# Performance work log

Hardware: AMD Instinct MI355X
Metric: run time of the kernel (lower is better)

Reference implementation:

```python
import jax, jax.numpy as jnp
import numpy as np

BN_EPS = 1e-5


def setup_inputs() -> dict:
    key = jax.random.key(0)
    ks = jax.random.split(key, 8)
    b, c, h, w, d = 16, 256, 128, 128, 64
    x = jax.random.normal(ks[0], (b, c, h, w), dtype=jnp.float32)
    conv1_w = jax.random.normal(ks[1], (c, c), dtype=jnp.float32) * np.sqrt(2.0 / c)
    conv1_b = jax.random.normal(ks[2], (c,), dtype=jnp.float32) * 0.02
    mk_w = jax.random.normal(ks[3], (d, c), dtype=jnp.float32) * np.sqrt(2.0 / d)
    mv_w = jnp.transpose(mk_w)  # original ties mv.weight = mk.weight.permute(1,0,2)
    conv2_w = jax.random.normal(ks[4], (c, c), dtype=jnp.float32) * np.sqrt(2.0 / c)
    bn_gamma = jnp.ones((c,), dtype=jnp.float32)
    bn_beta = jnp.zeros((c,), dtype=jnp.float32)
    bn_mean = jax.random.normal(ks[5], (c,), dtype=jnp.float32) * 0.1
    bn_var = jax.random.uniform(ks[6], (c,), dtype=jnp.float32, minval=0.5, maxval=1.5)
    return {"x": x, "conv1_w": conv1_w, "conv1_b": conv1_b, "mk_w": mk_w,
            "mv_w": mv_w, "conv2_w": conv2_w, "bn_gamma": bn_gamma,
            "bn_beta": bn_beta, "bn_mean": bn_mean, "bn_var": bn_var}


def reference(x, conv1_w, conv1_b, mk_w, mv_w, conv2_w, bn_gamma, bn_beta, bn_mean, bn_var):
    b, c, h, w = x.shape
    n = h * w
    identity = x
    # conv1: 1x1 conv with bias -> [b, c, n]
    y = jnp.einsum('oc,bchw->bohw', conv1_w, x) + conv1_b[None, :, None, None]
    y = y.reshape(b, c, n)
    # external attention: mk projection [b, d, n]
    attn = jnp.einsum('dc,bcn->bdn', mk_w, y)
    attn = jax.nn.softmax(attn, axis=-1)              # softmax over spatial N
    attn = attn / (1e-9 + attn.sum(axis=1, keepdims=True))  # column-normalize over d
    # mv projection back to channels [b, c, n]
    z = jnp.einsum('cd,bdn->bcn', mv_w, attn)
    z = z.reshape(b, c, h, w)
    # conv2 (1x1, no bias) + BatchNorm (inference) + residual + relu
    z = jnp.einsum('oc,bchw->bohw', conv2_w, z)
    inv = bn_gamma / jnp.sqrt(bn_var + BN_EPS)
    z = z * inv[None, :, None, None] + (bn_beta - bn_mean * inv)[None, :, None, None]
    return jax.nn.relu(z + identity)
```

## Files before the change

### kernel.cpp

```cpp
#include <hip/hip_runtime.h>
#include <hip/hip_bf16.h>

#define HW 16384
#define C  256
#define D  64
#define NB 16
#define M0 16.0f

typedef unsigned short u16;
typedef __attribute__((ext_vector_type(4))) float  f32x4;
typedef __attribute__((ext_vector_type(4))) short  s16x4;
typedef __attribute__((ext_vector_type(8))) short  s16x8;

__device__ __forceinline__ float bf2f(u16 u) {
    return __uint_as_float(((unsigned int)u) << 16);
}
__device__ __forceinline__ short f2bfs(float f) {
    union { __hip_bfloat16 h; short s; } u;
    u.h = __float2bfloat16(f);
    return u.s;
}
__device__ __forceinline__ u16 f2bf(float f) {
    unsigned int u = __float_as_uint(f);
    unsigned int r = (u + 0x7fffu + ((u >> 16) & 1u)) >> 16;
    return (u16)r;
}

#define MFMA16(a, b, c) __builtin_amdgcn_mfma_f32_16x16x32_bf16((a), (b), (c), 0, 0, 0)

__global__ void precompute_kernel(const float* __restrict__ conv1_w,
                                  const float* __restrict__ conv1_b,
                                  const float* __restrict__ mk_w,
                                  const float* __restrict__ mv_w,
                                  const float* __restrict__ conv2_w,
                                  const float* __restrict__ gamma,
                                  const float* __restrict__ beta,
                                  const float* __restrict__ mean,
                                  const float* __restrict__ var,
                                  short* __restrict__ Ath,
                                  short* __restrict__ Atl,
                                  float* __restrict__ amk,
                                  short* __restrict__ Bmb,
                                  float* __restrict__ shift,
                                  float* __restrict__ esum)
{
    int gid = blockIdx.x * blockDim.x + threadIdx.x;
    if (gid < C * D) {
        int d = gid >> 8, cp = gid & 255;
        float s = 0.f;
        for (int c = 0; c < C; ++c) s += mk_w[d * C + c] * conv1_w[c * C + cp];
        u16 h = f2bf(s);
        Ath[gid] = (short)h;
        Atl[gid] = (short)f2bf(s - bf2f(h));
    } else if (gid < 2 * C * D) {
        int g = gid - C * D;
        int o = g >> 6, d = g & 63;
        float inv = gamma[o] * rsqrtf(var[o] + 1e-5f);
        float s = 0.f;
        for (int c = 0; c < C; ++c) s += conv2_w[o * C + c] * mv_w[c * D + d];
        Bmb[g] = (short)f2bf(s * inv);
    } else if (gid < 2 * C * D + D) {
        int d = gid - 2 * C * D;
        float s = 0.f;
        for (int c = 0; c < C; ++c) s += mk_w[d * C + c] * conv1_b[c];
        amk[d] = s;
    } else if (gid < 2 * C * D + D + C) {
        int o = gid - (2 * C * D + D);
        float inv = gamma[o] * rsqrtf(var[o] + 1e-5f);
        shift[o] = beta[o] - mean[o] * inv;
    } else if (gid < 2 * C * D + D + C + NB * D) {
        esum[gid - (2 * C * D + D + C)] = 0.f;
    }
}

#define NT1 64
#define XR  (C + 8)
__global__ __launch_bounds__(256, 3) void pexp_kernel(const float* __restrict__ x,
                                                      const short* __restrict__ Ath,
                                                      const short* __restrict__ Atl,
                                                      const float* __restrict__ amk,
                                                      u16* __restrict__ pexp,
                                                      float* __restrict__ esum)
{
    __shared__ short xs[NT1 * XR];
    const int t = threadIdx.x;
    const int b = blockIdx.y;
    const int n0 = blockIdx.x * NT1;
    const int lane = t & 63, w = t >> 6;
    const int col = lane & 15, g = lane >> 4;

    const float* xb = x + (size_t)b * C * HW + n0;
    #pragma unroll
    for (int i = 0; i < 4; ++i) {
        int cell = i * 256 + t;
        int nq = cell & 15, cq = cell >> 4;
        int c0 = cq * 4, nn = nq * 4;
        const float* gp = xb + (size_t)c0 * HW + nn;
        f32x4 r0 = *(const f32x4*)(gp);
        f32x4 r1 = *(const f32x4*)(gp + HW);
        f32x4 r2 = *(const f32x4*)(gp + 2 * HW);
        f32x4 r3 = *(const f32x4*)(gp + 3 * HW);
        #pragma unroll
        for (int j = 0; j < 4; ++j) {
            s16x4 hi = { f2bfs(r0[j]), f2bfs(r1[j]), f2bfs(r2[j]), f2bfs(r3[j]) };
            *(s16x4*)&xs[(nn + j) * XR + c0] = hi;
        }
    }
    __syncthreads();

    s16x8 Ah[8], Al[8];
    {
        const short* ah = Ath + (size_t)(w * 16 + col) * C + 8 * g;
        const short* al = Atl + (size_t)(w * 16 + col) * C + 8 * g;
        #pragma unroll
        for (int ks = 0; ks < 8; ++ks) {
            Ah[ks] = *(const s16x8*)(ah + ks * 32);
            Al[ks] = *(const s16x8*)(al + ks * 32);
        }
    }

    f32x4 zz = {0.f, 0.f, 0.f, 0.f};
    f32x4 acc[4] = { zz, zz, zz, zz };
    #pragma unroll
    for (int ks = 0; ks < 8; ++ks) {
        #pragma unroll
        for (int nt = 0; nt < 4; ++nt) {
            s16x8 xf = *(const s16x8*)&xs[(nt * 16 + col) * XR + ks * 32 + 8 * g];
            acc[nt] = MFMA16(xf, Ah[ks], acc[nt]);
            acc[nt] = MFMA16(xf, Al[ks], acc[nt]);
        }
    }

    const float am = amk[w * 16 + col];
    u16* pb = pexp + (size_t)b * D * HW + (size_t)(w * 16 + col) * HW + n0;
    float rs = 0.f;
    #pragma unroll
    for (int nt = 0; nt < 4; ++nt) {
        s16x4 st4;
        #pragma unroll
        for (int r = 0; r < 4; ++r) {
            float e = exp2f((acc[nt][r] + am - M0) * 1.44269504088896340736f);
            rs += e;
            st4[r] = f2bfs(e);
        }
        *(s16x4*)(pb + nt * 16 + 4 * g) = st4;
    }
    rs += __shfl_xor(rs, 16);
    rs += __shfl_xor(rs, 32);
    if (lane < 16) atomicAdd(esum + b * D + w * 16 + lane, rs);
}

#define NT3 64
__global__ __launch_bounds__(256, 3) void out_kernel(const float* __restrict__ x,
                                                     const u16* __restrict__ pexp,
                                                     const float* __restrict__ esum,
                                                     const short* __restrict__ Bmb,
                                                     const float* __restrict__ shift,
                                                     float* __restrict__ out)
{
    __shared__ short ps[NT3 * 72];
    __shared__ float csum[4][NT3];
    __shared__ float rr[NT3];

    const int t = threadIdx.x;
    const int b  = (NB - 1) - blockIdx.y;
    const int n0 = ((int)gridDim.x - 1 - blockIdx.x) * NT3;

    {
        const int nl = t & 63, dq = t >> 6;
        const u16* lg = pexp + (size_t)b * D * HW + (size_t)(dq * 16) * HW + n0 + nl;
        const float* es = esum + b * D + dq * 16;
        float cs = 0.f;
        #pragma unroll
        for (int j4 = 0; j4 < 4; ++j4) {
            s16x4 pk;
            #pragma unroll
            for (int jj = 0; jj < 4; ++jj) {
                int j = j4 * 4 + jj;
                float iv = __fdividef(1.0f, es[j]);
                float pv = bf2f(lg[(size_t)j * HW]) * iv;
                cs += pv;
                pk[jj] = f2bfs(pv);
            }
            *(s16x4*)&ps[nl * 72 + dq * 16 + j4 * 4] = pk;
        }
        csum[dq][nl] = cs;
    }
    __syncthreads();
    if (t < NT3)
        rr[t] = __fdividef(1.0f, csum[0][t] + csum[1][t] + csum[2][t] + csum[3][t] + 1e-9f);
    __syncthreads();

    const int lane = t & 63, col = lane & 15, g = lane >> 4;
    const int w = t >> 6;

    s16x8 Bf[4][2];
    #pragma unroll
    for (int ot = 0; ot < 4; ++ot) {
        const short* bp = Bmb + (size_t)(w * 64 + ot * 16 + col) * D + 8 * g;
        Bf[ot][0] = *(const s16x8*)(bp);
        Bf[ot][1] = *(const s16x8*)(bp + 32);
    }

    f32x4 zz = {0.f, 0.f, 0.f, 0.f};
    f32x4 acc[4][4];
    #pragma unroll
    for (int ot = 0; ot < 4; ++ot)
        #pragma unroll
        for (int nt = 0; nt < 4; ++nt) acc[ot][nt] = zz;

    #pragma unroll
    for (int nt = 0; nt < 4; ++nt) {
        const short* pr = &ps[(nt * 16 + col) * 72 + 8 * g];
        s16x8 p0 = *(const s16x8*)(pr);
        s16x8 p1 = *(const s16x8*)(pr + 32);
        #pragma unroll
        for (int ot = 0; ot < 4; ++ot) {
            acc[ot][nt] = MFMA16(p0, Bf[ot][0], acc[ot][nt]);
            acc[ot][nt] = MFMA16(p1, Bf[ot][1], acc[ot][nt]);
        }
    }

    float sh[4];
    #pragma unroll
    for (int ot = 0; ot < 4; ++ot) sh[ot] = shift[w * 64 + ot * 16 + col];

    const float* xb = x + (size_t)b * C * HW + n0;
    float* ob = out + (size_t)b * C * HW + n0;
    #pragma unroll
    for (int nt = 0; nt < 4; ++nt) {
        f32x4 rv = *(const f32x4*)&rr[nt * 16 + 4 * g];
        #pragma unroll
        for (int ot = 0; ot < 4; ++ot) {
            const size_t off = (size_t)(w * 64 + ot * 16 + col) * HW + nt * 16 + 4 * g;
            f32x4 xv = *(const f32x4*)(xb + off);
            f32x4 vv;
            #pragma unroll
            for (int r = 0; r < 4; ++r)
                vv[r] = fmaxf(acc[ot][nt][r] * rv[r] + sh[ot] + xv[r], 0.f);
            __builtin_nontemporal_store(vv, (f32x4*)(ob + off));
        }
    }
}

extern "C" void kernel_launch(void* const* d_in, const int* in_sizes, int n_in,
                              void* d_out, int out_size, void* d_ws, size_t ws_size,
                              hipStream_t stream)
{
    const float* x       = (const float*)d_in[0];
    const float* conv1_w = (const float*)d_in[1];
    const float* conv1_b = (const float*)d_in[2];
    const float* mk_w    = (const float*)d_in[3];
    const float* mv_w    = (const float*)d_in[4];
    const float* conv2_w = (const float*)d_in[5];
    const float* gamma   = (const float*)d_in[6];
    const float* beta    = (const float*)d_in[7];
    const float* mean    = (const float*)d_in[8];
    const float* var     = (const float*)d_in[9];
    float* out = (float*)d_out;

    float* amk   = (float*)d_ws;
    float* shift = amk + D;
    float* esum  = shift + C;
    short* Ath   = (short*)(esum + NB * D);
    short* Atl   = Ath + C * D;
    short* Bmb   = Atl + C * D;
    u16* pexp    = (u16*)(Bmb + C * D);

    const int pre_work = 2 * C * D + D + C + NB * D;
    precompute_kernel<<<(pre_work + 255) / 256, 256, 0, stream>>>(
        conv1_w, conv1_b, mk_w, mv_w, conv2_w, gamma, beta, mean, var,
        Ath, Atl, amk, Bmb, shift, esum);

    pexp_kernel<<<dim3(HW / NT1, NB), 256, 0, stream>>>(x, Ath, Atl, amk, pexp, esum);

    out_kernel<<<dim3(HW / NT3, NB), 256, 0, stream>>>(x, pexp, esum, Bmb, shift, out);
}
```

Before: 544.2 us.

## Recompute attention logits in output kernel instead of materializing pexp buffer

```diff
diff --git a/kernel.cpp b/kernel.cpp
--- a/kernel.cpp
+++ b/kernel.cpp
@@ -6,6 +6,7 @@
 #define D  64
 #define NB 16
 #define M0 16.0f
+#define LOG2E 1.44269504088896340736f
 
 typedef unsigned short u16;
 typedef __attribute__((ext_vector_type(4))) float  f32x4;
@@ -75,11 +76,10 @@
 
 #define NT1 64
 #define XR  (C + 8)
-__global__ __launch_bounds__(256, 3) void pexp_kernel(const float* __restrict__ x,
+__global__ __launch_bounds__(256, 3) void esum_kernel(const float* __restrict__ x,
                                                       const short* __restrict__ Ath,
                                                       const short* __restrict__ Atl,
                                                       const float* __restrict__ amk,
-                                                      u16* __restrict__ pexp,
                                                       float* __restrict__ esum)
 {
     __shared__ short xs[NT1 * XR];
@@ -132,19 +132,12 @@
     }
 
     const float am = amk[w * 16 + col];
-    u16* pb = pexp + (size_t)b * D * HW + (size_t)(w * 16 + col) * HW + n0;
     float rs = 0.f;
     #pragma unroll
-    for (int nt = 0; nt < 4; ++nt) {
-        s16x4 st4;
-        #pragma unroll
-        for (int r = 0; r < 4; ++r) {
-            float e = exp2f((acc[nt][r] + am - M0) * 1.44269504088896340736f);
-            rs += e;
-            st4[r] = f2bfs(e);
-        }
-        *(s16x4*)(pb + nt * 16 + 4 * g) = st4;
-    }
+    for (int nt = 0; nt < 4; ++nt)
+        #pragma unroll
+        for (int r = 0; r < 4; ++r)
+            rs += exp2f((acc[nt][r] + am - M0) * LOG2E);
     rs += __shfl_xor(rs, 16);
     rs += __shfl_xor(rs, 32);
     if (lane < 16) atomicAdd(esum + b * D + w * 16 + lane, rs);
@@ -152,12 +145,15 @@
 
 #define NT3 64
 __global__ __launch_bounds__(256, 3) void out_kernel(const float* __restrict__ x,
-                                                     const u16* __restrict__ pexp,
+                                                     const short* __restrict__ Ath,
+                                                     const short* __restrict__ Atl,
+                                                     const float* __restrict__ amk,
                                                      const float* __restrict__ esum,
                                                      const short* __restrict__ Bmb,
                                                      const float* __restrict__ shift,
                                                      float* __restrict__ out)
 {
+    __shared__ short xs[NT3 * XR];
     __shared__ short ps[NT3 * 72];
     __shared__ float csum[4][NT3];
     __shared__ float rr[NT3];
@@ -165,34 +161,76 @@
     const int t = threadIdx.x;
     const int b  = (NB - 1) - blockIdx.y;
     const int n0 = ((int)gridDim.x - 1 - blockIdx.x) * NT3;
+    const int lane = t & 63, w = t >> 6;
+    const int col = lane & 15, g = lane >> 4;
+
+    const float* xb = x + (size_t)b * C * HW + n0;
+    #pragma unroll
+    for (int i = 0; i < 4; ++i) {
+        int cell = i * 256 + t;
+        int nq = cell & 15, cq = cell >> 4;
+        int c0 = cq * 4, nn = nq * 4;
+        const float* gp = xb + (size_t)c0 * HW + nn;
+        f32x4 r0 = *(const f32x4*)(gp);
+        f32x4 r1 = *(const f32x4*)(gp + HW);
+        f32x4 r2 = *(const f32x4*)(gp + 2 * HW);
+        f32x4 r3 = *(const f32x4*)(gp + 3 * HW);
+        #pragma unroll
+        for (int j = 0; j < 4; ++j) {
+            s16x4 hi = { f2bfs(r0[j]), f2bfs(r1[j]), f2bfs(r2[j]), f2bfs(r3[j]) };
+            *(s16x4*)&xs[(nn + j) * XR + c0] = hi;
+        }
+    }
+    __syncthreads();
+
+    {
+        s16x8 Ah[8], Al[8];
+        const short* ah = Ath + (size_t)(w * 16 + col) * C + 8 * g;
+        const short* al = Atl + (size_t)(w * 16 + col) * C + 8 * g;
+        #pragma unroll
+        for (int ks = 0; ks < 8; ++ks) {
+            Ah[ks] = *(const s16x8*)(ah + ks * 32);
+            Al[ks] = *(const s16x8*)(al + ks * 32);
+        }
+
+        f32x4 zz = {0.f, 0.f, 0.f, 0.f};
+        f32x4 acc[4] = { zz, zz, zz, zz };
+        #pragma unroll
+        for (int ks = 0; ks < 8; ++ks) {
+            #pragma unroll
+            for (int nt = 0; nt < 4; ++nt) {
+                s16x8 xf = *(const s16x8*)&xs[(nt * 16 + col) * XR + ks * 32 + 8 * g];
+                acc[nt] = MFMA16(xf, Ah[ks], acc[nt]);
+                acc[nt] = MFMA16(xf, Al[ks], acc[nt]);
+            }
+        }
+
+        const float am  = amk[w * 16 + col];
+        const float inv = __fdividef(1.0f, esum[b * D + w * 16 + col]);
+        #pragma unroll
+        for (int nt = 0; nt < 4; ++nt)
+            #pragma unroll
+            for (int r = 0; r < 4; ++r) {
+                float e = exp2f((acc[nt][r] + am - M0) * LOG2E);
+                ps[(nt * 16 + 4 * g + r) * 72 + w * 16 + col] = f2bfs(e * inv);
+            }
+    }
+    __syncthreads();
 
     {
         const int nl = t & 63, dq = t >> 6;
-        const u16* lg = pexp + (size_t)b * D * HW + (size_t)(dq * 16) * HW + n0 + nl;
-        const float* es = esum + b * D + dq * 16;
+        const short* pr = &ps[nl * 72 + dq * 16];
+        s16x8 a0 = *(const s16x8*)(pr);
+        s16x8 a1 = *(const s16x8*)(pr + 8);
         float cs = 0.f;
         #pragma unroll
-        for (int j4 = 0; j4 < 4; ++j4) {
-            s16x4 pk;
-            #pragma unroll
-            for (int jj = 0; jj < 4; ++jj) {
-                int j = j4 * 4 + jj;
-                float iv = __fdividef(1.0f, es[j]);
-                float pv = bf2f(lg[(size_t)j * HW]) * iv;
-                cs += pv;
-                pk[jj] = f2bfs(pv);
-            }
-            *(s16x4*)&ps[nl * 72 + dq * 16 + j4 * 4] = pk;
-        }
+        for (int k = 0; k < 8; ++k) cs += bf2f((u16)a0[k]) + bf2f((u16)a1[k]);
         csum[dq][nl] = cs;
     }
     __syncthreads();
     if (t < NT3)
         rr[t] = __fdividef(1.0f, csum[0][t] + csum[1][t] + csum[2][t] + csum[3][t] + 1e-9f);
     __syncthreads();
-
-    const int lane = t & 63, col = lane & 15, g = lane >> 4;
-    const int w = t >> 6;
 
     s16x8 Bf[4][2];
     #pragma unroll
@@ -225,7 +263,6 @@
     #pragma unroll
     for (int ot = 0; ot < 4; ++ot) sh[ot] = shift[w * 64 + ot * 16 + col];
 
-    const float* xb = x + (size_t)b * C * HW + n0;
     float* ob = out + (size_t)b * C * HW + n0;
     #pragma unroll
     for (int nt = 0; nt < 4; ++nt) {
@@ -265,14 +302,14 @@
     short* Ath   = (short*)(esum + NB * D);
     short* Atl   = Ath + C * D;
     short* Bmb   = Atl + C * D;
-    u16* pexp    = (u16*)(Bmb + C * D);
 
     const int pre_work = 2 * C * D + D + C + NB * D;
     precompute_kernel<<<(pre_work + 255) / 256, 256, 0, stream>>>(
         conv1_w, conv1_b, mk_w, mv_w, conv2_w, gamma, beta, mean, var,
         Ath, Atl, amk, Bmb, shift, esum);
 
-    pexp_kernel<<<dim3(HW / NT1, NB), 256, 0, stream>>>(x, Ath, Atl, amk, pexp, esum);
-
-    out_kernel<<<dim3(HW / NT3, NB), 256, 0, stream>>>(x, pexp, esum, Bmb, shift, out);
-}
+    esum_kernel<<<dim3(HW / NT1, NB), 256, 0, stream>>>(x, Ath, Atl, amk, esum);
+
+    out_kernel<<<dim3(HW / NT3, NB), 256, 0, stream>>>(x, Ath, Atl, amk, esum,
+                                                       Bmb, shift, out);
+}
```

After: 578.6 us. 6.3% more time.
